# Kernel optimization log

Hardware: AMD Instinct MI355X
Metric: run time of the kernel (lower is better)

The kernel has to match this reference:

```python
import jax, jax.numpy as jnp
import numpy as np

OUT_C, IN_C, KS, KN = 256, 256, 3, 4
TEMP = 1.0
D1 = OUT_C * KS            # 768
D2 = IN_C * KS             # 768
D2R = D2 // 2 + 1          # 385 (rfft width)


def _freq_indices():
    # mirror torch get_fft2freq(d1, d2, use_rfft=True)
    fh = np.fft.fftfreq(D1)
    fw = np.fft.rfftfreq(D2)
    grid = np.stack(np.meshgrid(fh, fw, indexing='ij'), axis=-1)  # (D1, D2R, 2)
    dist = np.linalg.norm(grid, axis=-1).ravel()
    idx = np.argsort(dist, kind='stable')
    return (idx // D2R).astype(np.int32), (idx % D2R).astype(np.int32)


def setup_inputs() -> dict:
    key = jax.random.key(0)
    k1, k2, k3 = jax.random.split(key, 3)
    b, h, w = 8, 64, 64
    fh, fw = _freq_indices()
    num_freq = fh.shape[0]  # 295680 = D1 * D2R (param_reduction == 1.0)
    return {
        'x': jax.random.normal(k1, (b, IN_C, h, w), dtype=jnp.float32),
        'dft_weight': jax.random.normal(k2, (KN, num_freq, 2), dtype=jnp.float32) * 1e-6,
        'k_att': jax.random.normal(k3, (b, KN, 1, 1), dtype=jnp.float32),
        'freq_h': jnp.asarray(fh),
        'freq_w': jnp.asarray(fw),
    }


def reference(x, dft_weight, k_att, freq_h, freq_w):
    b, c, h, w = x.shape
    # kernel attention: sigmoid(att / temp) * 2 / kernel_num
    att = jax.nn.sigmoid(k_att / TEMP) * (2.0 / KN)          # (b, KN, 1, 1)
    # weighted sum of per-kernel frequency weights -> (b, F, 2)
    wsum = jnp.einsum('knf,bk->bnf', dft_weight, att.reshape(b, KN))
    wc = jax.lax.complex(wsum[..., 0], wsum[..., 1])          # (b, F) complex
    # scatter into dense rfft2 map (indices are a permutation: no duplicates)
    dft_map = jnp.zeros((b, D1, D2R), dtype=jnp.complex64)
    dft_map = dft_map.at[:, freq_h, freq_w].set(wc)
    # inverse rFFT2 -> spatial weights (b, D1, D2)
    sw = jnp.fft.irfft2(dft_map, s=(D1, D2))
    # (b, out, ks, in, ks) -> (b, out, in, ks, ks) -> grouped-conv kernel
    wk = sw.reshape(b, OUT_C, KS, IN_C, KS).transpose(0, 1, 3, 2, 4)
    wk = wk.reshape(b * OUT_C, IN_C, KS, KS)
    # batch of per-sample convs == one grouped conv with groups=b
    xg = x.reshape(1, b * c, h, w)
    out = jax.lax.conv_general_dilated(
        xg, wk, window_strides=(1, 1), padding=[(1, 1), (1, 1)],
        dimension_numbers=('NCHW', 'OIHW', 'NCHW'), feature_group_count=b)
    return out.reshape(b, OUT_C, out.shape[2], out.shape[3])
```

## Files before the change

kernel.cpp:

```cpp
#include <hip/hip_runtime.h>
#include <math.h>

#define D1 768
#define D2R 385
#define NF 295680
#define KNUM 4
#define NB 8
#define NC 256
#define TWOPI_768 0.008181230868723419f

#define ATW_U32 1572864u
#define YA_U32 2752512u
#define T_U32 3981312u
#define SPECB_K_U32 344064u
#define WBF_BYTE 9437184u

typedef __attribute__((ext_vector_type(8))) short short8;
typedef __attribute__((ext_vector_type(16))) float f32x16;
union U4S8 { unsigned int u[4]; uint4 u4; short8 s8; };

static __device__ __forceinline__ unsigned int f2bf(float f) {
  unsigned int u = __float_as_uint(f);
  return (u + 0x7fffu + ((u >> 16) & 1u)) >> 16;
}

__global__ __launch_bounds__(256) void prep_kernel(
    const float* __restrict__ dw, const int* __restrict__ fh,
    const int* __restrict__ fw, unsigned int* __restrict__ ws) {
  long i = (long)blockIdx.x * 256 + threadIdx.x;
  if (i < 1182720) {
    int k = (int)(i / NF);
    int r = (int)(i - (long)k * NF);
    const float2 v = ((const float2*)dw)[i];
    int h = fh[r], c = fw[r];
    ws[(size_t)k * SPECB_K_U32 + (size_t)c * 768 + h] =
        f2bf(v.x) | (f2bf(v.y) << 16);
    return;
  }
  long j = i - 1182720;
  if (j < 1179648) {
    int ri = (int)(j / 589824);
    int rem = (int)(j - (long)ri * 589824);
    int m = rem / 768, h = rem - (rem / 768) * 768;
    int idx = (h * m) % 768;
    float s, c;
    sincosf((float)idx * TWOPI_768, &s, &c);
    unsigned lo, hi;
    if (ri == 0) { lo = f2bf(c); hi = f2bf(-s); }
    else         { lo = f2bf(s); hi = f2bf(c); }
    ws[ATW_U32 + j] = lo | (hi << 16);
  } else if (j < 1486848) {
    long p = j - 1179648;
    int n = (int)(p / 400), cc = (int)(p - (p / 400) * 400);
    unsigned v = 0;
    if (cc <= 384) {
      float wgt = (cc == 0 || cc == 384) ? 1.6954210069444445e-6f
                                         : 3.390842013888889e-6f;
      int idx = (cc * n) % 768;
      float s, c;
      sincosf((float)idx * TWOPI_768, &s, &c);
      v = f2bf(wgt * c) | (f2bf(-wgt * s) << 16);
    }
    ws[T_U32 + (size_t)n * 400 + cc] = v;
  } else if (j < 1680384) {
    long p = j - 1486848;
    int k = (int)(p / 48384);
    long r = p - (long)k * 48384;
    int row = 385 + (int)(r / 768);
    int col = (int)(r - (r / 768) * 768);
    ws[(size_t)k * SPECB_K_U32 + (size_t)row * 768 + col] = 0u;
  } else if (j < 1726464) {
    long p = j - 1680384;
    int k = (int)(p / 11520);
    long r = p - (long)k * 11520;
    int m = (int)(r / 15), jj = (int)(r - (r / 15) * 15);
    ws[YA_U32 + (size_t)k * 307200 + (size_t)m * 400 + 385 + jj] = 0u;
  }
}

__global__ __launch_bounds__(256) void fftA_kernel(
    const unsigned short* __restrict__ Atw,
    const unsigned short* __restrict__ specB,
    unsigned short* __restrict__ Ya) {
  __shared__ unsigned short Al[64 * 36], Bl[64 * 36];
  int t = threadIdx.x;
  int mt = blockIdx.x, nt = blockIdx.y, z = blockIdx.z;
  int ri = z & 1, k = z >> 1;
  const unsigned short* Ag =
      Atw + (size_t)ri * 1179648 + (size_t)(mt * 64) * 1536;
  const unsigned short* Bg =
      specB + (size_t)k * 688128 + (size_t)(nt * 64) * 1536;
  int rowS = t >> 2, q = t & 3;
  int lane = t & 63, w = t >> 6;
  int moff = (w & 1) * 32, noff = (w >> 1) * 32;
  int lm = lane & 31, half = lane >> 5;

  f32x16 acc;
#pragma unroll
  for (int r = 0; r < 16; ++r) acc[r] = 0.f;

  for (int kb = 0; kb < 48; ++kb) {
    uint4 av = *(const uint4*)(Ag + (size_t)rowS * 1536 + kb * 32 + q * 8);
    uint4 bv = *(const uint4*)(Bg + (size_t)rowS * 1536 + kb * 32 + q * 8);
    __syncthreads();
    int wr = rowS * 36 + q * 8;
    *(uint2*)&Al[wr] = make_uint2(av.x, av.y);
    *(uint2*)&Al[wr + 4] = make_uint2(av.z, av.w);
    *(uint2*)&Bl[wr] = make_uint2(bv.x, bv.y);
    *(uint2*)&Bl[wr + 4] = make_uint2(bv.z, bv.w);
    __syncthreads();
#pragma unroll
    for (int kk2 = 0; kk2 < 2; ++kk2) {
      int ab = (moff + lm) * 36 + kk2 * 16 + half * 8;
      int bb = (noff + lm) * 36 + kk2 * 16 + half * 8;
      U4S8 ua, ub;
      *(uint2*)&ua.u[0] = *(const uint2*)&Al[ab];
      *(uint2*)&ua.u[2] = *(const uint2*)&Al[ab + 4];
      *(uint2*)&ub.u[0] = *(const uint2*)&Bl[bb];
      *(uint2*)&ub.u[2] = *(const uint2*)&Bl[bb + 4];
      acc = __builtin_amdgcn_mfma_f32_32x32x16_bf16(ua.s8, ub.s8, acc, 0, 0, 0);
    }
  }

  int c = nt * 64 + noff + lm;
  if (c < D2R) {
    unsigned short* Yk = Ya + (size_t)k * 614400;
    int mb = mt * 64 + moff + 4 * half;
#pragma unroll
    for (int reg = 0; reg < 16; ++reg) {
      int m = mb + (reg & 3) + 8 * (reg >> 2);
      Yk[(size_t)m * 800 + 2 * c + ri] = (unsigned short)f2bf(acc[reg]);
    }
  }
}

__global__ __launch_bounds__(256) void fftB_kernel(
    const unsigned short* __restrict__ Ya, const unsigned short* __restrict__ T,
    float* __restrict__ SW) {
  __shared__ unsigned short Al[64 * 36], Bl[64 * 36];
  int t = threadIdx.x;
  int mt = blockIdx.x, nt = blockIdx.y, k = blockIdx.z;
  const unsigned short* Ag = Ya + (size_t)k * 614400 + (size_t)(mt * 64) * 800;
  const unsigned short* Bg = T + (size_t)(nt * 64) * 800;
  int rowS = t >> 2, q = t & 3;
  int lane = t & 63, w = t >> 6;
  int moff = (w & 1) * 32, noff = (w >> 1) * 32;
  int lm = lane & 31, half = lane >> 5;

  f32x16 acc;
#pragma unroll
  for (int r = 0; r < 16; ++r) acc[r] = 0.f;

  for (int kb = 0; kb < 25; ++kb) {
    uint4 av = *(const uint4*)(Ag + (size_t)rowS * 800 + kb * 32 + q * 8);
    uint4 bv = *(const uint4*)(Bg + (size_t)rowS * 800 + kb * 32 + q * 8);
    __syncthreads();
    int wr = rowS * 36 + q * 8;
    *(uint2*)&Al[wr] = make_uint2(av.x, av.y);
    *(uint2*)&Al[wr + 4] = make_uint2(av.z, av.w);
    *(uint2*)&Bl[wr] = make_uint2(bv.x, bv.y);
    *(uint2*)&Bl[wr + 4] = make_uint2(bv.z, bv.w);
    __syncthreads();
#pragma unroll
    for (int kk2 = 0; kk2 < 2; ++kk2) {
      int ab = (moff + lm) * 36 + kk2 * 16 + half * 8;
      int bb = (noff + lm) * 36 + kk2 * 16 + half * 8;
      U4S8 ua, ub;
      *(uint2*)&ua.u[0] = *(const uint2*)&Al[ab];
      *(uint2*)&ua.u[2] = *(const uint2*)&Al[ab + 4];
      *(uint2*)&ub.u[0] = *(const uint2*)&Bl[bb];
      *(uint2*)&ub.u[2] = *(const uint2*)&Bl[bb + 4];
      acc = __builtin_amdgcn_mfma_f32_32x32x16_bf16(ua.s8, ub.s8, acc, 0, 0, 0);
    }
  }

  float* SWk = SW + (size_t)k * 589824;
  int n = nt * 64 + noff + lm;
  int mb = mt * 64 + moff + 4 * half;
#pragma unroll
  for (int reg = 0; reg < 16; ++reg) {
    int m = mb + (reg & 3) + 8 * (reg >> 2);
    SWk[(size_t)m * 768 + n] = acc[reg];
  }
}

__global__ __launch_bounds__(256) void wprep_kernel(
    const float* __restrict__ ka, const float* __restrict__ SW,
    unsigned short* __restrict__ wBF) {
  int task = blockIdx.x * 256 + threadIdx.x;
  int oc = task & 255;
  int rest = task >> 8;
  int icb = rest & 15;
  int s = rest >> 4;
  int dy = s / 3, dx = s - dy * 3;

  float att[8][4];
#pragma unroll
  for (int b = 0; b < 8; ++b)
#pragma unroll
    for (int k = 0; k < 4; ++k)
      att[b][k] = 0.5f / (1.f + expf(-ka[b * 4 + k]));

  const float* r0 = SW + ((size_t)(oc * 3 + dy)) * D1 + icb * 48 + dx;
  const float* r1 = r0 + 589824;
  const float* r2 = r1 + 589824;
  const float* r3 = r2 + 589824;
  float v0[16], v1[16], v2[16], v3[16];
#pragma unroll
  for (int i = 0; i < 16; ++i) {
    v0[i] = r0[i * 3]; v1[i] = r1[i * 3];
    v2[i] = r2[i * 3]; v3[i] = r3[i * 3];
  }
#pragma unroll
  for (int b = 0; b < 8; ++b) {
    unsigned short ov[16];
#pragma unroll
    for (int i = 0; i < 16; ++i) {
      float v = att[b][0] * v0[i] + att[b][1] * v1[i] + att[b][2] * v2[i] +
                att[b][3] * v3[i];
      ov[i] = (unsigned short)f2bf(v);
    }
    uint4* dst =
        (uint4*)(wBF + ((((size_t)(b * 9 + s) * 16 + icb) * 256 + oc) * 16));
    dst[0] = *(uint4*)&ov[0];
    dst[1] = *(uint4*)&ov[8];
  }
}

__global__ __launch_bounds__(256, 2) void conv_mfma_kernel(
    const float* __restrict__ x, const unsigned short* __restrict__ wBF,
    float* __restrict__ out) {
  __shared__ __align__(16) unsigned char ldsX[4 * 66 * 48];
  int t = threadIdx.x;
  int pxt = blockIdx.x, oct = blockIdx.y, b = blockIdx.z;
  int py0 = pxt * 2;
  int oc0 = oct * 128;
  int lane = t & 63, w = t >> 6;
  int ocq = w >> 1, pxq = w & 1;
  int n = lane & 31, half = lane >> 5;

  if (t < 96) {
    int site = t / 12, word = t - site * 12;
    int r = site >> 1, c = (site & 1) ? 65 : 0;
    *(unsigned int*)(ldsX + (r * 66 + c) * 48 + word * 4) = 0u;
  }

  f32x16 acc[2][2];
#pragma unroll
  for (int i = 0; i < 2; ++i)
#pragma unroll
    for (int j = 0; j < 2; ++j)
#pragma unroll
      for (int r = 0; r < 16; ++r) acc[i][j][r] = 0.f;

  int s_cq = t >> 5, s_r = (t >> 3) & 3, s_icp = t & 7;
  int iy = py0 - 1 + s_r;
  bool valid = (iy >= 0 && iy < 64);
  const float* xpb =
      x + (((size_t)b * NC) * 64 + (valid ? iy : 0)) * 64 + s_cq * 8;
  unsigned char* xw = ldsX + (s_r * 66 + 1 + s_cq * 8) * 48 + s_icp * 4;

  const uint4* wg4 = (const uint4*)wBF;
  int laneoff = (oc0 + ocq * 64 + n) * 2 + half;

  U4S8 a0, a1, na0, na1;
  {
    size_t sb = ((size_t)(b * 9 + 0) * 16 + 0) * 512;
    a0.u4 = wg4[sb + laneoff];
    a1.u4 = wg4[sb + laneoff + 64];
  }

  for (int icb = 0; icb < 16; ++icb) {
    __syncthreads();
    {
      int ic = icb * 16 + s_icp * 2;
      float4 qa0 = make_float4(0.f, 0.f, 0.f, 0.f), qa1 = qa0, qb0 = qa0,
             qb1 = qa0;
      if (valid) {
        const float* p0 = xpb + (size_t)ic * 4096;
        qa0 = *(const float4*)p0;
        qa1 = *(const float4*)(p0 + 4);
        qb0 = *(const float4*)(p0 + 4096);
        qb1 = *(const float4*)(p0 + 4100);
      }
      float av[8] = {qa0.x, qa0.y, qa0.z, qa0.w, qa1.x, qa1.y, qa1.z, qa1.w};
      float bv[8] = {qb0.x, qb0.y, qb0.z, qb0.w, qb1.x, qb1.y, qb1.z, qb1.w};
#pragma unroll
      for (int j = 0; j < 8; ++j)
        *(unsigned int*)(xw + j * 48) = f2bf(av[j]) | (f2bf(bv[j]) << 16);
    }
    __syncthreads();
#pragma unroll
    for (int s = 0; s < 9; ++s) {
      bool pf = !(icb == 15 && s == 8);
      int ns = (s == 8) ? 0 : s + 1;
      int nicb = (s == 8) ? icb + 1 : icb;
      if (pf) {
        size_t sb = ((size_t)(b * 9 + ns) * 16 + nicb) * 512;
        na0.u4 = wg4[sb + laneoff];
        na1.u4 = wg4[sb + laneoff + 64];
      }
      int dy = s / 3, dx = s - dy * 3;
      const unsigned char* bb =
          ldsX + ((pxq + dy) * 66 + n + dx) * 48 + half * 16;
      short8 B0 = *(const short8*)bb;
      short8 B1 = *(const short8*)(bb + 32 * 48);
      acc[0][0] = __builtin_amdgcn_mfma_f32_32x32x16_bf16(a0.s8, B0, acc[0][0], 0, 0, 0);
      acc[0][1] = __builtin_amdgcn_mfma_f32_32x32x16_bf16(a0.s8, B1, acc[0][1], 0, 0, 0);
      acc[1][0] = __builtin_amdgcn_mfma_f32_32x32x16_bf16(a1.s8, B0, acc[1][0], 0, 0, 0);
      acc[1][1] = __builtin_amdgcn_mfma_f32_32x32x16_bf16(a1.s8, B1, acc[1][1], 0, 0, 0);
      a0 = na0;
      a1 = na1;
    }
  }

  int py = py0 + pxq;
#pragma unroll
  for (int osub = 0; osub < 2; ++osub)
#pragma unroll
    for (int psub = 0; psub < 2; ++psub) {
      int OC = oc0 + ocq * 64 + osub * 32 + 4 * half;
      int pxc = psub * 32 + n;
      float* op = out + (((size_t)(b * NC + OC)) * 64 + py) * 64 + pxc;
#pragma unroll
      for (int reg = 0; reg < 16; ++reg) {
        int ocm = (reg & 3) + 8 * (reg >> 2);
        op[(size_t)ocm * 4096] = acc[osub][psub][reg];
      }
    }
}

extern "C" void kernel_launch(void* const* d_in, const int* in_sizes, int n_in,
                              void* d_out, int out_size, void* d_ws,
                              size_t ws_size, hipStream_t stream) {
  const float* x = (const float*)d_in[0];
  const float* dw = (const float*)d_in[1];
  const float* ka = (const float*)d_in[2];
  const int* fh = (const int*)d_in[3];
  const int* fw = (const int*)d_in[4];
  float* out = (float*)d_out;
  unsigned int* ws = (unsigned int*)d_ws;
  const unsigned short* specB = (const unsigned short*)d_ws;
  const unsigned short* Atw = (const unsigned short*)((char*)d_ws + 6291456);
  unsigned short* Ya = (unsigned short*)((char*)d_ws + 11010048);
  const unsigned short* T = (const unsigned short*)((char*)d_ws + 15925248);
  float* SW = (float*)d_ws;
  unsigned short* wBF = (unsigned short*)((char*)d_ws + WBF_BYTE);

  hipLaunchKernelGGL(prep_kernel, dim3(11364), dim3(256), 0, stream, dw, fh,
                     fw, ws);
  hipLaunchKernelGGL(fftA_kernel, dim3(12, 7, 8), dim3(256), 0, stream, Atw,
                     specB, Ya);
  hipLaunchKernelGGL(fftB_kernel, dim3(12, 12, KNUM), dim3(256), 0, stream, Ya,
                     T, SW);
  hipLaunchKernelGGL(wprep_kernel, dim3(144), dim3(256), 0, stream, ka, SW,
                     wBF);
  hipLaunchKernelGGL(conv_mfma_kernel, dim3(32, 2, NB), dim3(256), 0, stream,
                     x, wBF, out);
}
```

Before: 221.2 us.

## Double-buffer LDS in FFT GEMMs and conv, deepen weight prefetch

```diff
diff --git a/kernel.cpp b/kernel.cpp
--- a/kernel.cpp
+++ b/kernel.cpp
@@ -82,7 +82,7 @@
     const unsigned short* __restrict__ Atw,
     const unsigned short* __restrict__ specB,
     unsigned short* __restrict__ Ya) {
-  __shared__ unsigned short Al[64 * 36], Bl[64 * 36];
+  __shared__ __align__(16) unsigned short Al[2][64 * 40], Bl[2][64 * 40];
   int t = threadIdx.x;
   int mt = blockIdx.x, nt = blockIdx.y, z = blockIdx.z;
   int ri = z & 1, k = z >> 1;
@@ -94,32 +94,39 @@
   int lane = t & 63, w = t >> 6;
   int moff = (w & 1) * 32, noff = (w >> 1) * 32;
   int lm = lane & 31, half = lane >> 5;
+  int wr = rowS * 40 + q * 8;
+  int ao = (moff + lm) * 40 + half * 8;
+  int bo = (noff + lm) * 40 + half * 8;
 
   f32x16 acc;
 #pragma unroll
   for (int r = 0; r < 16; ++r) acc[r] = 0.f;
 
+  uint4 av = *(const uint4*)(Ag + (size_t)rowS * 1536 + q * 8);
+  uint4 bv = *(const uint4*)(Bg + (size_t)rowS * 1536 + q * 8);
+  *(uint4*)&Al[0][wr] = av;
+  *(uint4*)&Bl[0][wr] = bv;
+  __syncthreads();
+
   for (int kb = 0; kb < 48; ++kb) {
-    uint4 av = *(const uint4*)(Ag + (size_t)rowS * 1536 + kb * 32 + q * 8);
-    uint4 bv = *(const uint4*)(Bg + (size_t)rowS * 1536 + kb * 32 + q * 8);
+    bool more = (kb < 47);
+    if (more) {
+      av = *(const uint4*)(Ag + (size_t)rowS * 1536 + (kb + 1) * 32 + q * 8);
+      bv = *(const uint4*)(Bg + (size_t)rowS * 1536 + (kb + 1) * 32 + q * 8);
+    }
+    const unsigned short* Ab = Al[kb & 1];
+    const unsigned short* Bb = Bl[kb & 1];
+#pragma unroll
+    for (int kk2 = 0; kk2 < 2; ++kk2) {
+      short8 a8 = *(const short8*)&Ab[ao + kk2 * 16];
+      short8 b8 = *(const short8*)&Bb[bo + kk2 * 16];
+      acc = __builtin_amdgcn_mfma_f32_32x32x16_bf16(a8, b8, acc, 0, 0, 0);
+    }
+    if (more) {
+      *(uint4*)&Al[(kb + 1) & 1][wr] = av;
+      *(uint4*)&Bl[(kb + 1) & 1][wr] = bv;
+    }
     __syncthreads();
-    int wr = rowS * 36 + q * 8;
-    *(uint2*)&Al[wr] = make_uint2(av.x, av.y);
-    *(uint2*)&Al[wr + 4] = make_uint2(av.z, av.w);
-    *(uint2*)&Bl[wr] = make_uint2(bv.x, bv.y);
-    *(uint2*)&Bl[wr + 4] = make_uint2(bv.z, bv.w);
-    __syncthreads();
-#pragma unroll
-    for (int kk2 = 0; kk2 < 2; ++kk2) {
-      int ab = (moff + lm) * 36 + kk2 * 16 + half * 8;
-      int bb = (noff + lm) * 36 + kk2 * 16 + half * 8;
-      U4S8 ua, ub;
-      *(uint2*)&ua.u[0] = *(const uint2*)&Al[ab];
-      *(uint2*)&ua.u[2] = *(const uint2*)&Al[ab + 4];
-      *(uint2*)&ub.u[0] = *(const uint2*)&Bl[bb];
-      *(uint2*)&ub.u[2] = *(const uint2*)&Bl[bb + 4];
-      acc = __builtin_amdgcn_mfma_f32_32x32x16_bf16(ua.s8, ub.s8, acc, 0, 0, 0);
-    }
   }
 
   int c = nt * 64 + noff + lm;
@@ -137,7 +144,7 @@
 __global__ __launch_bounds__(256) void fftB_kernel(
     const unsigned short* __restrict__ Ya, const unsigned short* __restrict__ T,
     float* __restrict__ SW) {
-  __shared__ unsigned short Al[64 * 36], Bl[64 * 36];
+  __shared__ __align__(16) unsigned short Al[2][64 * 40], Bl[2][64 * 40];
   int t = threadIdx.x;
   int mt = blockIdx.x, nt = blockIdx.y, k = blockIdx.z;
   const unsigned short* Ag = Ya + (size_t)k * 614400 + (size_t)(mt * 64) * 800;
@@ -146,32 +153,39 @@
   int lane = t & 63, w = t >> 6;
   int moff = (w & 1) * 32, noff = (w >> 1) * 32;
   int lm = lane & 31, half = lane >> 5;
+  int wr = rowS * 40 + q * 8;
+  int ao = (moff + lm) * 40 + half * 8;
+  int bo = (noff + lm) * 40 + half * 8;
 
   f32x16 acc;
 #pragma unroll
   for (int r = 0; r < 16; ++r) acc[r] = 0.f;
 
+  uint4 av = *(const uint4*)(Ag + (size_t)rowS * 800 + q * 8);
+  uint4 bv = *(const uint4*)(Bg + (size_t)rowS * 800 + q * 8);
+  *(uint4*)&Al[0][wr] = av;
+  *(uint4*)&Bl[0][wr] = bv;
+  __syncthreads();
+
   for (int kb = 0; kb < 25; ++kb) {
-    uint4 av = *(const uint4*)(Ag + (size_t)rowS * 800 + kb * 32 + q * 8);
-    uint4 bv = *(const uint4*)(Bg + (size_t)rowS * 800 + kb * 32 + q * 8);
+    bool more = (kb < 24);
+    if (more) {
+      av = *(const uint4*)(Ag + (size_t)rowS * 800 + (kb + 1) * 32 + q * 8);
+      bv = *(const uint4*)(Bg + (size_t)rowS * 800 + (kb + 1) * 32 + q * 8);
+    }
+    const unsigned short* Ab = Al[kb & 1];
+    const unsigned short* Bb = Bl[kb & 1];
+#pragma unroll
+    for (int kk2 = 0; kk2 < 2; ++kk2) {
+      short8 a8 = *(const short8*)&Ab[ao + kk2 * 16];
+      short8 b8 = *(const short8*)&Bb[bo + kk2 * 16];
+      acc = __builtin_amdgcn_mfma_f32_32x32x16_bf16(a8, b8, acc, 0, 0, 0);
+    }
+    if (more) {
+      *(uint4*)&Al[(kb + 1) & 1][wr] = av;
+      *(uint4*)&Bl[(kb + 1) & 1][wr] = bv;
+    }
     __syncthreads();
-    int wr = rowS * 36 + q * 8;
-    *(uint2*)&Al[wr] = make_uint2(av.x, av.y);
-    *(uint2*)&Al[wr + 4] = make_uint2(av.z, av.w);
-    *(uint2*)&Bl[wr] = make_uint2(bv.x, bv.y);
-    *(uint2*)&Bl[wr + 4] = make_uint2(bv.z, bv.w);
-    __syncthreads();
-#pragma unroll
-    for (int kk2 = 0; kk2 < 2; ++kk2) {
-      int ab = (moff + lm) * 36 + kk2 * 16 + half * 8;
-      int bb = (noff + lm) * 36 + kk2 * 16 + half * 8;
-      U4S8 ua, ub;
-      *(uint2*)&ua.u[0] = *(const uint2*)&Al[ab];
-      *(uint2*)&ua.u[2] = *(const uint2*)&Al[ab + 4];
-      *(uint2*)&ub.u[0] = *(const uint2*)&Bl[bb];
-      *(uint2*)&ub.u[2] = *(const uint2*)&Bl[bb + 4];
-      acc = __builtin_amdgcn_mfma_f32_32x32x16_bf16(ua.s8, ub.s8, acc, 0, 0, 0);
-    }
   }
 
   float* SWk = SW + (size_t)k * 589824;
@@ -221,7 +235,7 @@
       ov[i] = (unsigned short)f2bf(v);
     }
     uint4* dst =
-        (uint4*)(wBF + ((((size_t)(b * 9 + s) * 16 + icb) * 256 + oc) * 16));
+        (uint4*)(wBF + ((((size_t)(b * 16 + icb) * 9 + s) * 256 + oc) * 16));
     dst[0] = *(uint4*)&ov[0];
     dst[1] = *(uint4*)&ov[8];
   }
@@ -230,19 +244,19 @@
 __global__ __launch_bounds__(256, 2) void conv_mfma_kernel(
     const float* __restrict__ x, const unsigned short* __restrict__ wBF,
     float* __restrict__ out) {
-  __shared__ __align__(16) unsigned char ldsX[4 * 66 * 48];
+  __shared__ __align__(16) unsigned char ldsX[2][4 * 66 * 48];
   int t = threadIdx.x;
   int pxt = blockIdx.x, oct = blockIdx.y, b = blockIdx.z;
-  int py0 = pxt * 2;
-  int oc0 = oct * 128;
+  int py0 = pxt * 2, oc0 = oct * 128;
   int lane = t & 63, w = t >> 6;
   int ocq = w >> 1, pxq = w & 1;
   int n = lane & 31, half = lane >> 5;
 
-  if (t < 96) {
-    int site = t / 12, word = t - site * 12;
+  if (t < 192) {
+    int buf = t / 96, r2 = t - buf * 96;
+    int site = r2 / 12, word = r2 - site * 12;
     int r = site >> 1, c = (site & 1) ? 65 : 0;
-    *(unsigned int*)(ldsX + (r * 66 + c) * 48 + word * 4) = 0u;
+    *(unsigned int*)(&ldsX[buf][(r * 66 + c) * 48 + word * 4]) = 0u;
   }
 
   f32x16 acc[2][2];
@@ -258,60 +272,79 @@
   bool valid = (iy >= 0 && iy < 64);
   const float* xpb =
       x + (((size_t)b * NC) * 64 + (valid ? iy : 0)) * 64 + s_cq * 8;
-  unsigned char* xw = ldsX + (s_r * 66 + 1 + s_cq * 8) * 48 + s_icp * 4;
+  int xwoff = (s_r * 66 + 1 + s_cq * 8) * 48 + s_icp * 4;
 
   const uint4* wg4 = (const uint4*)wBF;
-  int laneoff = (oc0 + ocq * 64 + n) * 2 + half;
-
-  U4S8 a0, a1, na0, na1;
+  size_t abase =
+      (size_t)b * 144 * 512 + (size_t)(oc0 + ocq * 64 + n) * 2 + half;
+  U4S8 pf[3][2];
+#pragma unroll
+  for (int i = 0; i < 3; ++i) {
+    pf[i][0].u4 = wg4[abase + (size_t)i * 512];
+    pf[i][1].u4 = wg4[abase + (size_t)i * 512 + 64];
+  }
+
   {
-    size_t sb = ((size_t)(b * 9 + 0) * 16 + 0) * 512;
-    a0.u4 = wg4[sb + laneoff];
-    a1.u4 = wg4[sb + laneoff + 64];
-  }
+    float4 qa0 = make_float4(0.f, 0.f, 0.f, 0.f), qa1 = qa0, qb0 = qa0,
+           qb1 = qa0;
+    if (valid) {
+      const float* p0 = xpb + (size_t)(s_icp * 2) * 4096;
+      qa0 = *(const float4*)p0;
+      qa1 = *(const float4*)(p0 + 4);
+      qb0 = *(const float4*)(p0 + 4096);
+      qb1 = *(const float4*)(p0 + 4100);
+    }
+    float av[8] = {qa0.x, qa0.y, qa0.z, qa0.w, qa1.x, qa1.y, qa1.z, qa1.w};
+    float bv[8] = {qb0.x, qb0.y, qb0.z, qb0.w, qb1.x, qb1.y, qb1.z, qb1.w};
+    unsigned char* xw = &ldsX[0][0] + xwoff;
+#pragma unroll
+    for (int j = 0; j < 8; ++j)
+      *(unsigned int*)(xw + j * 48) = f2bf(av[j]) | (f2bf(bv[j]) << 16);
+  }
+  __syncthreads();
 
   for (int icb = 0; icb < 16; ++icb) {
-    __syncthreads();
-    {
-      int ic = icb * 16 + s_icp * 2;
-      float4 qa0 = make_float4(0.f, 0.f, 0.f, 0.f), qa1 = qa0, qb0 = qa0,
-             qb1 = qa0;
-      if (valid) {
-        const float* p0 = xpb + (size_t)ic * 4096;
-        qa0 = *(const float4*)p0;
-        qa1 = *(const float4*)(p0 + 4);
-        qb0 = *(const float4*)(p0 + 4096);
-        qb1 = *(const float4*)(p0 + 4100);
+    float4 qa0 = make_float4(0.f, 0.f, 0.f, 0.f), qa1 = qa0, qb0 = qa0,
+           qb1 = qa0;
+    if (icb < 15 && valid) {
+      const float* p0 = xpb + ((size_t)(icb + 1) * 16 + s_icp * 2) * 4096;
+      qa0 = *(const float4*)p0;
+      qa1 = *(const float4*)(p0 + 4);
+      qb0 = *(const float4*)(p0 + 4096);
+      qb1 = *(const float4*)(p0 + 4100);
+    }
+    const unsigned char* bufR = &ldsX[icb & 1][0];
+#pragma unroll
+    for (int s = 0; s < 9; ++s) {
+      int step = icb * 9 + s;
+      int slot = s % 3;
+      int dy = s / 3, dx = s - dy * 3;
+      const unsigned char* bb =
+          bufR + ((pxq + dy) * 66 + n + dx) * 48 + half * 16;
+      short8 B0 = *(const short8*)bb;
+      short8 B1 = *(const short8*)(bb + 32 * 48);
+      acc[0][0] = __builtin_amdgcn_mfma_f32_32x32x16_bf16(pf[slot][0].s8, B0,
+                                                          acc[0][0], 0, 0, 0);
+      acc[0][1] = __builtin_amdgcn_mfma_f32_32x32x16_bf16(pf[slot][0].s8, B1,
+                                                          acc[0][1], 0, 0, 0);
+      acc[1][0] = __builtin_amdgcn_mfma_f32_32x32x16_bf16(pf[slot][1].s8, B0,
+                                                          acc[1][0], 0, 0, 0);
+      acc[1][1] = __builtin_amdgcn_mfma_f32_32x32x16_bf16(pf[slot][1].s8, B1,
+                                                          acc[1][1], 0, 0, 0);
+      if (step + 3 < 144) {
+        pf[slot][0].u4 = wg4[abase + (size_t)(step + 3) * 512];
+        pf[slot][1].u4 = wg4[abase + (size_t)(step + 3) * 512 + 64];
       }
+    }
+    if (icb < 15) {
       float av[8] = {qa0.x, qa0.y, qa0.z, qa0.w, qa1.x, qa1.y, qa1.z, qa1.w};
       float bv[8] = {qb0.x, qb0.y, qb0.z, qb0.w, qb1.x, qb1.y, qb1.z, qb1.w};
+      unsigned char* xw = &ldsX[(icb + 1) & 1][0] + xwoff;
 #pragma unroll
       for (int j = 0; j < 8; ++j)
         *(unsigned int*)(xw + j * 48) = f2bf(av[j]) | (f2bf(bv[j]) << 16);
     }
     __syncthreads();
-#pragma unroll
-    for (int s = 0; s < 9; ++s) {
-      bool pf = !(icb == 15 && s == 8);
-      int ns = (s == 8) ? 0 : s + 1;
-      int nicb = (s == 8) ? icb + 1 : icb;
-      if (pf) {
-        size_t sb = ((size_t)(b * 9 + ns) * 16 + nicb) * 512;
-        na0.u4 = wg4[sb + laneoff];
-        na1.u4 = wg4[sb + laneoff + 64];
-      }
-      int dy = s / 3, dx = s - dy * 3;
-      const unsigned char* bb =
-          ldsX + ((pxq + dy) * 66 + n + dx) * 48 + half * 16;
-      short8 B0 = *(const short8*)bb;
-      short8 B1 = *(const short8*)(bb + 32 * 48);
-      acc[0][0] = __builtin_amdgcn_mfma_f32_32x32x16_bf16(a0.s8, B0, acc[0][0], 0, 0, 0);
-      acc[0][1] = __builtin_amdgcn_mfma_f32_32x32x16_bf16(a0.s8, B1, acc[0][1], 0, 0, 0);
-      acc[1][0] = __builtin_amdgcn_mfma_f32_32x32x16_bf16(a1.s8, B0, acc[1][0], 0, 0, 0);
-      acc[1][1] = __builtin_amdgcn_mfma_f32_32x32x16_bf16(a1.s8, B1, acc[1][1], 0, 0, 0);
-      a0 = na0;
-      a1 = na1;
-    }
   }
 
   int py = py0 + pxq;
```

Measured after the change: 201.1 us. -9.1%, faster.
